# Kernel tuning notes

Hardware: AMD Instinct MI355X
Metric: run time of the kernel (lower is better)

## Reference

```python
import jax, jax.numpy as jnp
import numpy as np

B, C, H, W = 32, 512, 56, 56
P = 64  # planes = C / ratio
EPS = 1e-3


def setup_inputs() -> dict:
    key = jax.random.key(0)
    ks = jax.random.split(key, 10)
    return {
        "x": jax.random.normal(ks[0], (B, C, H, W), jnp.float32),
        "wm": jax.random.normal(ks[1], (1, C), jnp.float32) * 0.05,
        "bm": jax.random.normal(ks[2], (1,), jnp.float32) * 0.05,
        "w1": jax.random.normal(ks[3], (P, C), jnp.float32) * 0.05,
        "b1": jax.random.normal(ks[4], (P,), jnp.float32) * 0.05,
        "ln_g": jax.random.normal(ks[5], (P,), jnp.float32) * 0.1 + 1.0,
        "ln_b": jax.random.normal(ks[6], (P,), jnp.float32) * 0.05,
        "w2": jax.random.normal(ks[7], (C, P), jnp.float32) * 0.05,
        "b2": jax.random.normal(ks[8], (C,), jnp.float32) * 0.05,
        "gamma": jax.random.normal(ks[9], (1,), jnp.float32) * 0.1,
    }


def reference(x, wm, bm, w1, b1, ln_g, ln_b, w2, b2, gamma):
    b, c, h, w = x.shape
    xf = x.reshape(b, c, h * w)                       # (B, C, S)
    # attention spatial pool: 1x1 conv mask -> softmax over spatial -> weighted sum
    mask = jnp.einsum('bcs,c->bs', xf, wm[0]) + bm[0]  # (B, S)
    attn = jax.nn.softmax(mask, axis=-1)               # softmax over H*W
    context = jnp.einsum('bcs,bs->bc', xf, attn)       # (B, C)
    # channel_add_conv: 1x1 conv -> LayerNorm([P,1,1], eps=1e-3) -> ReLU -> 1x1 conv
    hid = jnp.einsum('pc,bc->bp', w1, context) + b1    # (B, P)
    mu = hid.mean(axis=-1, keepdims=True)
    var = jnp.mean((hid - mu) ** 2, axis=-1, keepdims=True)
    hid = (hid - mu) / jnp.sqrt(var + EPS) * ln_g + ln_b
    hid = jax.nn.relu(hid)
    add = jnp.einsum('cp,bp->bc', w2, hid) + b2        # (B, C)
    return x + gamma[0] * add[:, :, None, None]
```

## Files before the change

kernel.cpp:

```cpp
#include <hip/hip_runtime.h>

constexpr int kB = 32;
constexpr int kC = 512;
constexpr int kS = 56 * 56;
constexpr int kP = 64;
constexpr float kEps = 1e-3f;

__global__ void k_mask(const float* __restrict__ x, const float* __restrict__ wm,
                       float* __restrict__ mask) {
    __shared__ float swm[kC];
    for (int c = threadIdx.x; c < kC; c += blockDim.x) swm[c] = wm[c];
    __syncthreads();

    const int b = blockIdx.y;
    const int s = blockIdx.x * blockDim.x + threadIdx.x;
    if (s >= kS) return;

    const float* xp = x + (size_t)b * kC * kS + s;
    float acc = 0.f;
#pragma unroll 8
    for (int c = 0; c < kC; ++c) acc += xp[(size_t)c * kS] * swm[c];
    mask[b * kS + s] = acc;
}

__global__ void k_softmax(float* __restrict__ mask) {
    const int b = blockIdx.x;
    float* m = mask + b * kS;
    const int tid  = threadIdx.x;
    const int lane = tid & 63;
    const int wave = tid >> 6;

    __shared__ float sred[4];
    __shared__ float sbc;

    float mx = -INFINITY;
    for (int s = tid; s < kS; s += blockDim.x) mx = fmaxf(mx, m[s]);
    for (int off = 32; off; off >>= 1) mx = fmaxf(mx, __shfl_down(mx, off));
    if (lane == 0) sred[wave] = mx;
    __syncthreads();
    if (tid == 0) {
        float v = sred[0];
        for (int i = 1; i < 4; ++i) v = fmaxf(v, sred[i]);
        sbc = v;
    }
    __syncthreads();
    mx = sbc;

    float sum = 0.f;
    for (int s = tid; s < kS; s += blockDim.x) {
        float e = expf(m[s] - mx);
        m[s] = e;
        sum += e;
    }
    for (int off = 32; off; off >>= 1) sum += __shfl_down(sum, off);
    if (lane == 0) sred[wave] = sum;
    __syncthreads();
    if (tid == 0) sbc = sred[0] + sred[1] + sred[2] + sred[3];
    __syncthreads();
    const float inv = 1.f / sbc;

    for (int s = tid; s < kS; s += blockDim.x) m[s] *= inv;
}

__global__ void k_context(const float* __restrict__ x, const float* __restrict__ attn,
                          float* __restrict__ context) {
    const int gwave = (int)((blockIdx.x * blockDim.x + threadIdx.x) >> 6);
    const int lane  = threadIdx.x & 63;
    if (gwave >= kB * kC) return;
    const int b = gwave / kC;

    const float4* xr = (const float4*)(x + (size_t)gwave * kS);
    const float4* ar = (const float4*)(attn + (size_t)b * kS);

    float acc = 0.f;
    for (int i = lane; i < kS / 4; i += 64) {
        float4 xv = xr[i];
        float4 av = ar[i];
        acc += xv.x * av.x + xv.y * av.y + xv.z * av.z + xv.w * av.w;
    }
    for (int off = 32; off; off >>= 1) acc += __shfl_down(acc, off);
    if (lane == 0) context[gwave] = acc;
}

__global__ void k_mlp(const float* __restrict__ context, const float* __restrict__ w1,
                      const float* __restrict__ b1, const float* __restrict__ ln_g,
                      const float* __restrict__ ln_b, const float* __restrict__ w2,
                      const float* __restrict__ b2, float* __restrict__ add) {
    const int b   = blockIdx.x;
    const int tid = threadIdx.x;

    __shared__ float ctx[kC];
    __shared__ float hid[kP];

    for (int c = tid; c < kC; c += 64) ctx[c] = context[b * kC + c];
    __syncthreads();

    float h = b1[tid];
    const float* w1p = w1 + tid * kC;
    for (int c = 0; c < kC; ++c) h += w1p[c] * ctx[c];

    float mu = h;
    for (int off = 32; off; off >>= 1) mu += __shfl_down(mu, off);
    mu = __shfl(mu, 0) * (1.f / kP);
    float d = h - mu;
    float var = d * d;
    for (int off = 32; off; off >>= 1) var += __shfl_down(var, off);
    var = __shfl(var, 0) * (1.f / kP);
    h = d * rsqrtf(var + kEps) * ln_g[tid] + ln_b[tid];
    h = fmaxf(h, 0.f);
    hid[tid] = h;
    __syncthreads();

    for (int c = tid; c < kC; c += 64) {
        float a = b2[c];
        const float* w2c = w2 + c * kP;
#pragma unroll
        for (int p = 0; p < kP; ++p) a += w2c[p] * hid[p];
        add[b * kC + c] = a;
    }
}

__global__ void k_out(const float* __restrict__ x, const float* __restrict__ add,
                      const float* __restrict__ gamma, float* __restrict__ out) {
    const size_t i4 = (size_t)blockIdx.x * blockDim.x + threadIdx.x;
    const size_t n4 = (size_t)kB * kC * kS / 4;
    if (i4 >= n4) return;
    const int bc = (int)(i4 / (kS / 4));
    const float a = gamma[0] * add[bc];
    float4 xv = ((const float4*)x)[i4];
    float4 o;
    o.x = xv.x + a; o.y = xv.y + a; o.z = xv.z + a; o.w = xv.w + a;
    ((float4*)out)[i4] = o;
}

extern "C" void kernel_launch(void* const* d_in, const int* in_sizes, int n_in,
                              void* d_out, int out_size, void* d_ws, size_t ws_size,
                              hipStream_t stream) {
    const float* x     = (const float*)d_in[0];
    const float* wm    = (const float*)d_in[1];
    const float* w1    = (const float*)d_in[3];
    const float* b1    = (const float*)d_in[4];
    const float* ln_g  = (const float*)d_in[5];
    const float* ln_b  = (const float*)d_in[6];
    const float* w2    = (const float*)d_in[7];
    const float* b2    = (const float*)d_in[8];
    const float* gamma = (const float*)d_in[9];
    float* out = (float*)d_out;

    float* ws      = (float*)d_ws;
    float* mask    = ws;
    float* context = mask + kB * kS;
    float* add     = context + kB * kC;

    k_mask<<<dim3((kS + 255) / 256, kB), 256, 0, stream>>>(x, wm, mask);
    k_softmax<<<kB, 256, 0, stream>>>(mask);
    k_context<<<(kB * kC) / 4, 256, 0, stream>>>(x, mask, context);
    k_mlp<<<kB, 64, 0, stream>>>(context, w1, b1, ln_g, ln_b, w2, b2, add);

    const size_t n4 = (size_t)kB * kC * kS / 4;
    k_out<<<(unsigned)((n4 + 255) / 256), 256, 0, stream>>>(x, add, gamma, out);
}
```

Baseline: 451.4 us.

## Fuse mask, softmax and context into one tiled pass with online-softmax partials

Replaces the separate mask, softmax and context kernels with one kernel that loads each 32-position spatial tile of x into shared memory once. From that tile it computes the mask logits, a local max and sum, and partial context vectors. A combine kernel merges the per-tile partials with rescaled exponentials (online softmax) and runs the MLP with all 512 threads. This removes one full read of x and the mask round-trips, at the cost of writing per-tile partial context to the workspace. The output kernel now uses nontemporal stores.

```diff
diff --git a/kernel.cpp b/kernel.cpp
--- a/kernel.cpp
+++ b/kernel.cpp
@@ -6,131 +6,166 @@
 constexpr int kP = 64;
 constexpr float kEps = 1e-3f;
 
-__global__ void k_mask(const float* __restrict__ x, const float* __restrict__ wm,
-                       float* __restrict__ mask) {
+constexpr int kST = 32;
+constexpr int kNB = kS / kST;
+constexpr int kPadC = kC + 1;
+
+typedef float f4v __attribute__((ext_vector_type(4)));
+
+__global__ __launch_bounds__(512)
+void k_fused_pass(const float* __restrict__ x, const float* __restrict__ wm,
+                  float* __restrict__ pc, float* __restrict__ pmz) {
+    __shared__ float xs[kST][kPadC];
     __shared__ float swm[kC];
-    for (int c = threadIdx.x; c < kC; c += blockDim.x) swm[c] = wm[c];
+    __shared__ float pm[16][kST];
+    __shared__ float es[kST];
+
+    const int b    = blockIdx.y;
+    const int tile = blockIdx.x;
+    const int s0   = tile * kST;
+    const int t    = threadIdx.x;
+
+    for (int c = t; c < kC; c += 512) swm[c] = wm[c];
+
+    const float* xb = x + (size_t)b * kC * kS + s0;
+    {
+        const int c0 = t >> 3;
+        const int si = t & 7;
+        for (int cc = 0; cc < kC; cc += 64) {
+            const int c = cc + c0;
+            f4v v = *(const f4v*)(xb + (size_t)c * kS + si * 4);
+            xs[si * 4 + 0][c] = v.x;
+            xs[si * 4 + 1][c] = v.y;
+            xs[si * 4 + 2][c] = v.z;
+            xs[si * 4 + 3][c] = v.w;
+        }
+    }
     __syncthreads();
 
-    const int b = blockIdx.y;
-    const int s = blockIdx.x * blockDim.x + threadIdx.x;
-    if (s >= kS) return;
-
-    const float* xp = x + (size_t)b * kC * kS + s;
-    float acc = 0.f;
+    {
+        const int s  = t & 31;
+        const int ch = t >> 5;
+        const int cb = ch * 32;
+        float acc = 0.f;
 #pragma unroll 8
-    for (int c = 0; c < kC; ++c) acc += xp[(size_t)c * kS] * swm[c];
-    mask[b * kS + s] = acc;
-}
-
-__global__ void k_softmax(float* __restrict__ mask) {
-    const int b = blockIdx.x;
-    float* m = mask + b * kS;
-    const int tid  = threadIdx.x;
-    const int lane = tid & 63;
-    const int wave = tid >> 6;
-
-    __shared__ float sred[4];
-    __shared__ float sbc;
-
-    float mx = -INFINITY;
-    for (int s = tid; s < kS; s += blockDim.x) mx = fmaxf(mx, m[s]);
-    for (int off = 32; off; off >>= 1) mx = fmaxf(mx, __shfl_down(mx, off));
-    if (lane == 0) sred[wave] = mx;
-    __syncthreads();
-    if (tid == 0) {
-        float v = sred[0];
-        for (int i = 1; i < 4; ++i) v = fmaxf(v, sred[i]);
-        sbc = v;
+        for (int i = 0; i < 32; ++i) acc += xs[s][cb + i] * swm[cb + i];
+        pm[ch][s] = acc;
     }
     __syncthreads();
-    mx = sbc;
 
-    float sum = 0.f;
-    for (int s = tid; s < kS; s += blockDim.x) {
-        float e = expf(m[s] - mx);
-        m[s] = e;
-        sum += e;
+    if (t < 64) {
+        float v = 0.f, m = -INFINITY;
+        if (t < kST) {
+#pragma unroll
+            for (int ch = 0; ch < 16; ++ch) v += pm[ch][t];
+            m = v;
+        }
+        float mx = m;
+        for (int off = 32; off; off >>= 1) mx = fmaxf(mx, __shfl_xor(mx, off));
+        const float e = (t < kST) ? expf(v - mx) : 0.f;
+        float sum = e;
+        for (int off = 32; off; off >>= 1) sum += __shfl_xor(sum, off);
+        if (t < kST) es[t] = e;
+        if (t == 0) {
+            pmz[(b * kNB + tile) * 2 + 0] = mx;
+            pmz[(b * kNB + tile) * 2 + 1] = sum;
+        }
     }
-    for (int off = 32; off; off >>= 1) sum += __shfl_down(sum, off);
-    if (lane == 0) sred[wave] = sum;
-    __syncthreads();
-    if (tid == 0) sbc = sred[0] + sred[1] + sred[2] + sred[3];
-    __syncthreads();
-    const float inv = 1.f / sbc;
-
-    for (int s = tid; s < kS; s += blockDim.x) m[s] *= inv;
-}
-
-__global__ void k_context(const float* __restrict__ x, const float* __restrict__ attn,
-                          float* __restrict__ context) {
-    const int gwave = (int)((blockIdx.x * blockDim.x + threadIdx.x) >> 6);
-    const int lane  = threadIdx.x & 63;
-    if (gwave >= kB * kC) return;
-    const int b = gwave / kC;
-
-    const float4* xr = (const float4*)(x + (size_t)gwave * kS);
-    const float4* ar = (const float4*)(attn + (size_t)b * kS);
-
-    float acc = 0.f;
-    for (int i = lane; i < kS / 4; i += 64) {
-        float4 xv = xr[i];
-        float4 av = ar[i];
-        acc += xv.x * av.x + xv.y * av.y + xv.z * av.z + xv.w * av.w;
-    }
-    for (int off = 32; off; off >>= 1) acc += __shfl_down(acc, off);
-    if (lane == 0) context[gwave] = acc;
-}
-
-__global__ void k_mlp(const float* __restrict__ context, const float* __restrict__ w1,
-                      const float* __restrict__ b1, const float* __restrict__ ln_g,
-                      const float* __restrict__ ln_b, const float* __restrict__ w2,
-                      const float* __restrict__ b2, float* __restrict__ add) {
-    const int b   = blockIdx.x;
-    const int tid = threadIdx.x;
-
-    __shared__ float ctx[kC];
-    __shared__ float hid[kP];
-
-    for (int c = tid; c < kC; c += 64) ctx[c] = context[b * kC + c];
     __syncthreads();
 
-    float h = b1[tid];
-    const float* w1p = w1 + tid * kC;
-    for (int c = 0; c < kC; ++c) h += w1p[c] * ctx[c];
-
-    float mu = h;
-    for (int off = 32; off; off >>= 1) mu += __shfl_down(mu, off);
-    mu = __shfl(mu, 0) * (1.f / kP);
-    float d = h - mu;
-    float var = d * d;
-    for (int off = 32; off; off >>= 1) var += __shfl_down(var, off);
-    var = __shfl(var, 0) * (1.f / kP);
-    h = d * rsqrtf(var + kEps) * ln_g[tid] + ln_b[tid];
-    h = fmaxf(h, 0.f);
-    hid[tid] = h;
-    __syncthreads();
-
-    for (int c = tid; c < kC; c += 64) {
-        float a = b2[c];
-        const float* w2c = w2 + c * kP;
-#pragma unroll
-        for (int p = 0; p < kP; ++p) a += w2c[p] * hid[p];
-        add[b * kC + c] = a;
+    {
+        float acc = 0.f;
+#pragma unroll 8
+        for (int s = 0; s < kST; ++s) acc += xs[s][t] * es[s];
+        pc[((size_t)b * kNB + tile) * kC + t] = acc;
     }
 }
 
-__global__ void k_out(const float* __restrict__ x, const float* __restrict__ add,
-                      const float* __restrict__ gamma, float* __restrict__ out) {
+__global__ __launch_bounds__(512)
+void k_combine_mlp(const float* __restrict__ pc, const float* __restrict__ pmz,
+                   const float* __restrict__ w1, const float* __restrict__ b1,
+                   const float* __restrict__ ln_g, const float* __restrict__ ln_b,
+                   const float* __restrict__ w2, const float* __restrict__ b2,
+                   float* __restrict__ add) {
+    const int b = blockIdx.x;
+    const int t = threadIdx.x;
+    __shared__ float scale[kNB];
+    __shared__ float ctx[kC];
+    __shared__ float hp[kP][9];
+    __shared__ float hid[kP];
+
+    if (t < 64) {
+        const float m1 = (t      < kNB) ? pmz[(b * kNB + t     ) * 2] : -INFINITY;
+        const float m2 = (t + 64 < kNB) ? pmz[(b * kNB + t + 64) * 2] : -INFINITY;
+        float m = fmaxf(m1, m2);
+        for (int off = 32; off; off >>= 1) m = fmaxf(m, __shfl_xor(m, off));
+        const float e1 = (t      < kNB) ? expf(m1 - m) : 0.f;
+        const float e2 = (t + 64 < kNB) ? expf(m2 - m) : 0.f;
+        float z = 0.f;
+        if (t      < kNB) z += pmz[(b * kNB + t     ) * 2 + 1] * e1;
+        if (t + 64 < kNB) z += pmz[(b * kNB + t + 64) * 2 + 1] * e2;
+        for (int off = 32; off; off >>= 1) z += __shfl_xor(z, off);
+        const float inv = 1.f / z;
+        if (t      < kNB) scale[t]      = e1 * inv;
+        if (t + 64 < kNB) scale[t + 64] = e2 * inv;
+    }
+    __syncthreads();
+
+    {
+        float acc = 0.f;
+        for (int i = 0; i < kNB; ++i)
+            acc += pc[((size_t)b * kNB + i) * kC + t] * scale[i];
+        ctx[t] = acc;
+    }
+    __syncthreads();
+
+    {
+        const int p = t & 63, k = t >> 6;
+        const float* w1p = w1 + p * kC + k * 64;
+        const float* cxp = ctx + k * 64;
+        float acc = 0.f;
+#pragma unroll 8
+        for (int i = 0; i < 64; ++i) acc += w1p[i] * cxp[i];
+        hp[p][k] = acc;
+    }
+    __syncthreads();
+
+    if (t < 64) {
+        float h = b1[t];
+#pragma unroll
+        for (int k = 0; k < 8; ++k) h += hp[t][k];
+        float mu = h;
+        for (int off = 32; off; off >>= 1) mu += __shfl_xor(mu, off);
+        mu *= (1.f / kP);
+        const float d = h - mu;
+        float var = d * d;
+        for (int off = 32; off; off >>= 1) var += __shfl_xor(var, off);
+        var *= (1.f / kP);
+        const float hv = d * rsqrtf(var + kEps) * ln_g[t] + ln_b[t];
+        hid[t] = fmaxf(hv, 0.f);
+    }
+    __syncthreads();
+
+    {
+        float a = b2[t];
+        const float* w2c = w2 + t * kP;
+#pragma unroll
+        for (int p = 0; p < kP; ++p) a += w2c[p] * hid[p];
+        add[b * kC + t] = a;
+    }
+}
+
+__global__ __launch_bounds__(256)
+void k_out(const float* __restrict__ x, const float* __restrict__ add,
+           const float* __restrict__ gamma, float* __restrict__ out) {
     const size_t i4 = (size_t)blockIdx.x * blockDim.x + threadIdx.x;
     const size_t n4 = (size_t)kB * kC * kS / 4;
     if (i4 >= n4) return;
     const int bc = (int)(i4 / (kS / 4));
     const float a = gamma[0] * add[bc];
-    float4 xv = ((const float4*)x)[i4];
-    float4 o;
-    o.x = xv.x + a; o.y = xv.y + a; o.z = xv.z + a; o.w = xv.w + a;
-    ((float4*)out)[i4] = o;
+    f4v xv = ((const f4v*)x)[i4];
+    f4v o = {xv.x + a, xv.y + a, xv.z + a, xv.w + a};
+    __builtin_nontemporal_store(o, (f4v*)out + i4);
 }
 
 extern "C" void kernel_launch(void* const* d_in, const int* in_sizes, int n_in,
@@ -147,15 +182,13 @@
     const float* gamma = (const float*)d_in[9];
     float* out = (float*)d_out;
 
-    float* ws      = (float*)d_ws;
-    float* mask    = ws;
-    float* context = mask + kB * kS;
-    float* add     = context + kB * kC;
+    float* ws  = (float*)d_ws;
+    float* pc  = ws;
+    float* pmz = pc + (size_t)kB * kNB * kC;
+    float* add = pmz + (size_t)kB * kNB * 2;
 
-    k_mask<<<dim3((kS + 255) / 256, kB), 256, 0, stream>>>(x, wm, mask);
-    k_softmax<<<kB, 256, 0, stream>>>(mask);
-    k_context<<<(kB * kC) / 4, 256, 0, stream>>>(x, mask, context);
-    k_mlp<<<kB, 64, 0, stream>>>(context, w1, b1, ln_g, ln_b, w2, b2, add);
+    k_fused_pass<<<dim3(kNB, kB), 512, 0, stream>>>(x, wm, pc, pmz);
+    k_combine_mlp<<<kB, 512, 0, stream>>>(pc, pmz, w1, b1, ln_g, ln_b, w2, b2, add);
 
     const size_t n4 = (size_t)kB * kC * kS / 4;
     k_out<<<(unsigned)((n4 + 255) / 256), 256, 0, stream>>>(x, add, gamma, out);
```

New measurement: 395.9 us. -12.3%, faster.
